# Performance work log

Hardware: AMD Instinct MI355X
Metric: run time of the kernel (lower is better)

## Reference

```python
import jax, jax.numpy as jnp
import numpy as np
import jax.lax as lax

KERNEL = 7
STRIDE = 1
PAD = 3

def setup_inputs() -> dict:
    key = jax.random.key(0)
    kx, kw = jax.random.split(key)
    x = jax.random.normal(kx, (64, 512, 512), dtype=jnp.float32)
    weight = jax.random.normal(kw, (KERNEL, KERNEL), dtype=jnp.float32)
    return {"x": x, "weight": weight}

def reference(x, weight):
    # x: [B, H, W] single-channel; weight: [k, k]
    # Original computes cross-correlation (no kernel flip) with zero padding.
    lhs = x[:, None, :, :]                      # [B, 1, H, W]
    rhs = weight[None, None, :, :]              # [O=1, I=1, k, k]
    out = lax.conv_general_dilated(
        lhs, rhs,
        window_strides=(STRIDE, STRIDE),
        padding=[(PAD, PAD), (PAD, PAD)],
        dimension_numbers=("NCHW", "OIHW", "NCHW"),
    )
    return out[:, 0, :, :]                      # [B, H_out, W_out]
```

## Files before the change

kernel.cpp:

```cpp
#include <hip/hip_runtime.h>
#include <stdint.h>


#define IMG_W 512
#define IMG_H 512
#define NIMG  64
#define TW    256
#define TH    16
#define HALO  3
#define LDS_W 264
#define LDS_H (TH + 2*HALO)

__device__ __forceinline__ void gload_lds16(const float* src, float* dst_lds)
{
    __builtin_amdgcn_global_load_lds(
        (__attribute__((address_space(1))) void*)(uintptr_t)src,
        (__attribute__((address_space(3))) void*)(uintptr_t)dst_lds,
        16, 0, 0);
}

__global__ __launch_bounds__(256, 6) void conv7x7_kernel(
    const float* __restrict__ x,
    const float* __restrict__ wgt,
    float* __restrict__ out)
{
    __shared__ float tile[LDS_H * LDS_W];

    const int tid  = threadIdx.x;
    const int wave = tid >> 6;
    const int lane = tid & 63;
    const int bx   = blockIdx.x * TW;
    const int by   = blockIdx.y * TH;
    const int n    = blockIdx.z;

    const float* img = x + (size_t)n * (IMG_W * IMG_H);

    float w[49];
    #pragma unroll
    for (int i = 0; i < 49; ++i) w[i] = wgt[i];

    for (int r = wave; r < LDS_H; r += 4) {
        const int gy = by - HALO + r;
        float* dst = &tile[r * LDS_W + 4 + 4 * lane];
        if ((unsigned)gy < IMG_H) {
            gload_lds16(&img[(size_t)gy * IMG_W + bx + 4 * lane], dst);
        } else {
            *(float4*)dst = make_float4(0.f, 0.f, 0.f, 0.f);
        }
    }

    if (tid < 2 * LDS_H) {
        const int r    = tid >> 1;
        const int side = tid & 1;
        const int cb   = side ? (LDS_W - 4) : 0;
        const int gx   = side ? (bx + 256) : (bx - 4);
        const int gy   = by - HALO + r;
        float4 v = make_float4(0.f, 0.f, 0.f, 0.f);
        if (((unsigned)gy < IMG_H) && ((unsigned)gx < IMG_W))
            v = *(const float4*)&img[(size_t)gy * IMG_W + gx];
        *(float4*)&tile[r * LDS_W + cb] = v;
    }

    __syncthreads();

    const int lx = lane * 4;
    const int rbase = wave * 4;

    float acc[4][4] = {};

    #pragma unroll
    for (int r = 0; r < 10; ++r) {
        const float* rowp = &tile[(rbase + r) * LDS_W + lx];
        const float4 a = *(const float4*)(rowp + 0);
        const float4 b = *(const float4*)(rowp + 4);
        const float4 c = *(const float4*)(rowp + 8);
        const float row[12] = {a.x, a.y, a.z, a.w,
                               b.x, b.y, b.z, b.w,
                               c.x, c.y, c.z, c.w};
        #pragma unroll
        for (int j = 0; j < 4; ++j) {
            const int ky = r - j;
            if (ky >= 0 && ky < 7) {
                #pragma unroll
                for (int kx = 0; kx < 7; ++kx) {
                    const float wv = w[ky * 7 + kx];
                    #pragma unroll
                    for (int cc = 0; cc < 4; ++cc)
                        acc[j][cc] = fmaf(row[1 + kx + cc], wv, acc[j][cc]);
                }
            }
        }
    }

    float* o = out + (size_t)n * (IMG_W * IMG_H);
    #pragma unroll
    for (int j = 0; j < 4; ++j) {
        float4 v = make_float4(acc[j][0], acc[j][1], acc[j][2], acc[j][3]);
        *(float4*)&o[(size_t)(by + rbase + j) * IMG_W + bx + lx] = v;
    }
}

extern "C" void kernel_launch(void* const* d_in, const int* in_sizes, int n_in,
                              void* d_out, int out_size, void* d_ws, size_t ws_size,
                              hipStream_t stream)
{
    const float* x   = (const float*)d_in[0];
    const float* wgt = (const float*)d_in[1];
    float* out       = (float*)d_out;

    dim3 grid(IMG_W / TW, IMG_H / TH, NIMG);
    conv7x7_kernel<<<grid, 256, 0, stream>>>(x, wgt, out);
}
```

Measured before the change: 123.9 us.

## Replace LDS tile staging with direct global loads per thread

Removes the shared-memory tile, the global_load_lds staging, the halo-column loads and the block barrier. Each thread now reads its 10 input rows (three float4 each) straight from global memory and depends on L1/L2 to serve the overlapping reuse between neighbouring threads and waves. The occupancy hint in launch_bounds drops from 6 to 4. The trade is more global/cache traffic in exchange for no LDS usage and no synchronisation.

```diff
diff --git a/kernel.cpp b/kernel.cpp
--- a/kernel.cpp
+++ b/kernel.cpp
@@ -7,25 +7,12 @@
 #define NIMG  64
 #define TW    256
 #define TH    16
-#define HALO  3
-#define LDS_W 264
-#define LDS_H (TH + 2*HALO)
 
-__device__ __forceinline__ void gload_lds16(const float* src, float* dst_lds)
-{
-    __builtin_amdgcn_global_load_lds(
-        (__attribute__((address_space(1))) void*)(uintptr_t)src,
-        (__attribute__((address_space(3))) void*)(uintptr_t)dst_lds,
-        16, 0, 0);
-}
-
-__global__ __launch_bounds__(256, 6) void conv7x7_kernel(
+__global__ __launch_bounds__(256, 4) void conv7x7_kernel(
     const float* __restrict__ x,
     const float* __restrict__ wgt,
     float* __restrict__ out)
 {
-    __shared__ float tile[LDS_H * LDS_W];
-
     const int tid  = threadIdx.x;
     const int wave = tid >> 6;
     const int lane = tid & 63;
@@ -34,46 +21,31 @@
     const int n    = blockIdx.z;
 
     const float* img = x + (size_t)n * (IMG_W * IMG_H);
+    float* o = out + (size_t)n * (IMG_W * IMG_H);
 
     float w[49];
     #pragma unroll
     for (int i = 0; i < 49; ++i) w[i] = wgt[i];
 
-    for (int r = wave; r < LDS_H; r += 4) {
-        const int gy = by - HALO + r;
-        float* dst = &tile[r * LDS_W + 4 + 4 * lane];
-        if ((unsigned)gy < IMG_H) {
-            gload_lds16(&img[(size_t)gy * IMG_W + bx + 4 * lane], dst);
-        } else {
-            *(float4*)dst = make_float4(0.f, 0.f, 0.f, 0.f);
-        }
-    }
+    const int lx = bx + lane * 4;
+    const int ry = by + wave * 4;
 
-    if (tid < 2 * LDS_H) {
-        const int r    = tid >> 1;
-        const int side = tid & 1;
-        const int cb   = side ? (LDS_W - 4) : 0;
-        const int gx   = side ? (bx + 256) : (bx - 4);
-        const int gy   = by - HALO + r;
-        float4 v = make_float4(0.f, 0.f, 0.f, 0.f);
-        if (((unsigned)gy < IMG_H) && ((unsigned)gx < IMG_W))
-            v = *(const float4*)&img[(size_t)gy * IMG_W + gx];
-        *(float4*)&tile[r * LDS_W + cb] = v;
-    }
-
-    __syncthreads();
-
-    const int lx = lane * 4;
-    const int rbase = wave * 4;
+    const bool has_left  = (lx != 0);
+    const bool has_right = (lx != IMG_W - 4);
 
     float acc[4][4] = {};
 
     #pragma unroll
     for (int r = 0; r < 10; ++r) {
-        const float* rowp = &tile[(rbase + r) * LDS_W + lx];
-        const float4 a = *(const float4*)(rowp + 0);
-        const float4 b = *(const float4*)(rowp + 4);
-        const float4 c = *(const float4*)(rowp + 8);
+        const int gy = ry - 3 + r;
+        float4 a = make_float4(0.f, 0.f, 0.f, 0.f);
+        float4 b = a, c = a;
+        if ((unsigned)gy < IMG_H) {
+            const float* rp = img + (size_t)gy * IMG_W + lx;
+            if (has_left)  a = *(const float4*)(rp - 4);
+            b = *(const float4*)rp;
+            if (has_right) c = *(const float4*)(rp + 4);
+        }
         const float row[12] = {a.x, a.y, a.z, a.w,
                                b.x, b.y, b.z, b.w,
                                c.x, c.y, c.z, c.w};
@@ -92,11 +64,10 @@
         }
     }
 
-    float* o = out + (size_t)n * (IMG_W * IMG_H);
     #pragma unroll
     for (int j = 0; j < 4; ++j) {
         float4 v = make_float4(acc[j][0], acc[j][1], acc[j][2], acc[j][3]);
-        *(float4*)&o[(size_t)(by + rbase + j) * IMG_W + bx + lx] = v;
+        *(float4*)&o[(size_t)(ry + j) * IMG_W + lx] = v;
     }
 }
 
```

After: 226.7 us. 83.0% more time.
